# Kernel optimization log

Hardware: AMD Instinct MI355X
Metric: run time of the kernel (lower is better)

## Reference

```python
import jax, jax.numpy as jnp
import numpy as np

C_IN = 256
C_BN = 64


def conv1x1(x, w, b):
    # x: [B, Cin, H, W], w: [Cout, Cin], b: [Cout] -> [B, Cout, H, W]
    return jnp.einsum('oc,bchw->bohw', w, x) + b[None, :, None, None]


def setup_inputs() -> dict:
    key = jax.random.key(0)
    ks = jax.random.split(key, 9)
    B, H, W = 4, 64, 64
    s_in = 1.0 / np.sqrt(C_IN)
    s_bn = 1.0 / np.sqrt(C_BN)
    return {
        'x': jax.random.normal(ks[0], (B, C_IN, H, W), jnp.float32),
        'w_k': jax.random.uniform(ks[1], (C_BN, C_IN), jnp.float32, -s_in, s_in),
        'b_k': jax.random.uniform(ks[2], (C_BN,), jnp.float32, -s_in, s_in),
        'w_q': jax.random.uniform(ks[3], (C_BN, C_IN), jnp.float32, -s_in, s_in),
        'b_q': jax.random.uniform(ks[4], (C_BN,), jnp.float32, -s_in, s_in),
        'w_v': jax.random.uniform(ks[5], (C_BN, C_IN), jnp.float32, -s_in, s_in),
        'b_v': jax.random.uniform(ks[6], (C_BN,), jnp.float32, -s_in, s_in),
        'w_u': jax.random.uniform(ks[7], (C_IN, C_BN), jnp.float32, -s_bn, s_bn),
        'b_u': jax.random.uniform(ks[8], (C_IN,), jnp.float32, -s_bn, s_bn),
    }


def reference(x, w_k, b_k, w_q, b_q, w_v, b_v, w_u, b_u):
    B, C, H, W = x.shape
    N = H * W
    xk = conv1x1(x, w_k, b_k).reshape(B, C_BN, N)            # [B, d, N]
    xq = conv1x1(x, w_q, b_q).reshape(B, C_BN, N)            # [B, d, N]
    xv = conv1x1(x, w_v, b_v).reshape(B, C_BN, N)            # [B, d, N]
    qk = jnp.einsum('bdi,bdk->bik', xq, xk)                  # [B, N, N]
    attn = jax.nn.softmax(qk, axis=2)                        # softmax over keys
    out = jnp.einsum('bik,bdk->bdi', attn, xv)               # [B, d, N]
    out = out.reshape(B, C_BN, H, W)
    y = conv1x1(out, w_u, b_u)                               # [B, C, H, W]
    return x + y
```

## Files before the change

### kernel.cpp

```cpp
#include <hip/hip_runtime.h>
#include <hip/hip_bf16.h>
#include <math.h>

#define N_TOK 4096
#define CIN 256
#define CBN 64
#define LOG2E 1.44269504f

typedef __attribute__((ext_vector_type(8))) short bf16x8;
typedef __attribute__((ext_vector_type(4))) float f32x4;

static __device__ __forceinline__ unsigned short f2bf(float f) {
    union { float f; unsigned u; } v; v.f = f;
    unsigned r = v.u + 0x7fffu + ((v.u >> 16) & 1u);
    return (unsigned short)(r >> 16);
}
static __device__ __forceinline__ unsigned pack2(float a, float b) {
    float2 t2; t2.x = a; t2.y = b;
    __hip_bfloat162 h = __float22bfloat162_rn(t2);
    union { __hip_bfloat162 h; unsigned u; } cv; cv.h = h;
    return cv.u;
}

__global__ __launch_bounds__(256) void prep_w(
        const float* __restrict__ wq, const float* __restrict__ wk,
        const float* __restrict__ wv, const float* __restrict__ wu,
        const float* __restrict__ bq,
        short* __restrict__ Wb, short* __restrict__ Wu, float* __restrict__ bqs) {
    int idx = blockIdx.x * 256 + threadIdx.x;
    int d = idx >> 8, c = idx & 255;
    Wb[d * 256 + c]         = (short)f2bf(wq[idx] * LOG2E);
    Wb[(64 + d) * 256 + c]  = (short)f2bf(wk[idx]);
    Wb[(128 + d) * 256 + c] = (short)f2bf(wv[idx]);
    Wu[idx] = (short)f2bf(wu[idx]);
    if (idx < 64) bqs[idx] = bq[idx] * LOG2E;
}

__global__ __launch_bounds__(256) void qkv_kernel(
        const float* __restrict__ x, const short* __restrict__ Wb,
        const float* __restrict__ bqs, const float* __restrict__ bk, const float* __restrict__ bv,
        short* __restrict__ Qt, short* __restrict__ Kt, short* __restrict__ Vd) {
    int t = threadIdx.x;
    int blk = blockIdx.x;
    int b = blk >> 7;
    int n0 = (blk & 127) * 32;

    __shared__ short Xs[32][264];

    {
        int tok4 = t & 7;
        int cb = t >> 3;
        const float* xb = x + (size_t)b * CIN * N_TOK + n0 + tok4 * 4;
        #pragma unroll
        for (int p = 0; p < 8; ++p) {
            int c = p * 32 + cb;
            float4 xv = *(const float4*)(xb + (size_t)c * N_TOK);
            float xs[4] = {xv.x, xv.y, xv.z, xv.w};
            #pragma unroll
            for (int i = 0; i < 4; ++i)
                Xs[tok4 * 4 + i][c] = (short)f2bf(xs[i]);
        }
    }
    __syncthreads();

    int w = t >> 6;
    int g = (t >> 4) & 3;
    int lr = t & 15;

    f32x4 acc[3][2];
    #pragma unroll
    for (int m = 0; m < 3; ++m)
        #pragma unroll
        for (int st = 0; st < 2; ++st) acc[m][st] = (f32x4){0.f, 0.f, 0.f, 0.f};
    const short* wbase = Wb + (size_t)(w * 16 + lr) * 256 + 8 * g;
    #pragma unroll
    for (int ks = 0; ks < 8; ++ks) {
        bf16x8 xf0 = *(const bf16x8*)&Xs[lr][ks * 32 + 8 * g];
        bf16x8 xf1 = *(const bf16x8*)&Xs[16 + lr][ks * 32 + 8 * g];
        #pragma unroll
        for (int m = 0; m < 3; ++m) {
            bf16x8 wf = *(const bf16x8*)(wbase + (size_t)m * 64 * 256 + ks * 32);
            acc[m][0] = __builtin_amdgcn_mfma_f32_16x16x32_bf16(wf, xf0, acc[m][0], 0, 0, 0);
            acc[m][1] = __builtin_amdgcn_mfma_f32_16x16x32_bf16(wf, xf1, acc[m][1], 0, 0, 0);
        }
    }
    int d0 = w * 16 + 4 * g;
    float4 bq4 = *(const float4*)(bqs + d0);
    float4 bk4 = *(const float4*)(bk + d0);
    float4 bv4 = *(const float4*)(bv + d0);
    float bvr[4] = {bv4.x, bv4.y, bv4.z, bv4.w};
    #pragma unroll
    for (int st = 0; st < 2; ++st) {
        int tok = n0 + st * 16 + lr;
        size_t qo = ((size_t)b * N_TOK + tok) * 64 + d0;
        uint2 qp, kp;
        qp.x = pack2(acc[0][st][0] + bq4.x, acc[0][st][1] + bq4.y);
        qp.y = pack2(acc[0][st][2] + bq4.z, acc[0][st][3] + bq4.w);
        kp.x = pack2(acc[1][st][0] + bk4.x, acc[1][st][1] + bk4.y);
        kp.y = pack2(acc[1][st][2] + bk4.z, acc[1][st][3] + bk4.w);
        *(uint2*)(Qt + qo) = qp;
        *(uint2*)(Kt + qo) = kp;
        int u = tok & 31;
        int vcol = (tok & ~31) + 8 * ((u >> 2) & 3) + 4 * (u >> 4) + (u & 3);
        #pragma unroll
        for (int r = 0; r < 4; ++r)
            Vd[((size_t)b * 64 + d0 + r) * N_TOK + vcol] = (short)f2bf(acc[2][st][r] + bvr[r]);
    }
}

__global__ __launch_bounds__(1024, 4) void attn_out_kernel(
        const short* __restrict__ Qt, const short* __restrict__ Kt,
        const short* __restrict__ Vsw, const short* __restrict__ Wu,
        const float* __restrict__ bu, const float* __restrict__ x,
        float* __restrict__ y) {
    int t = threadIdx.x;
    int w = t >> 6;
    int wq = w >> 3;
    int sp = w & 7;
    int g = (t >> 4) & 3;
    int lr = t & 15;
    int l = t & 63;

    int bid = blockIdx.x;
    int blk = ((bid & 7) << 5) | (bid >> 3);
    int b = blk >> 6;
    int q0 = (blk & 63) * 64;

    const short* Qb = Qt + (size_t)b * N_TOK * 64;
    const short* Kb = Kt + (size_t)b * N_TOK * 64;
    const short* Vb = Vsw + (size_t)b * 64 * N_TOK;

    __shared__ __align__(16) char LB[8][2][8192];
    __shared__ float Ml[32][16];
    __shared__ __align__(16) short Olds[64 * 64];

    bf16x8 qf[2][2];
    #pragma unroll
    for (int j = 0; j < 2; ++j) {
        const short* qp = Qb + (q0 + (wq * 2 + j) * 16 + lr) * 64 + 8 * g;
        qf[j][0] = *(const bf16x8*)qp;
        qf[j][1] = *(const bf16x8*)(qp + 32);
    }

    f32x4 o[2][4];
    #pragma unroll
    for (int j = 0; j < 2; ++j)
        #pragma unroll
        for (int mt = 0; mt < 4; ++mt) o[j][mt] = (f32x4){0.f, 0.f, 0.f, 0.f};
    float la0 = 0.f, la1 = 0.f;

    int krow = l >> 3;
    int kchk = ((l & 7) ^ krow) * 8;
    int vrow = l >> 2;
    int vchk = ((l & 3) ^ (vrow & 3)) * 8;

    auto STAGE = [&](int kt, int buf) {
        int k0s = sp * 512 + kt * 32;
        char* dst0 = &LB[sp][buf][0];
        if (wq == 0) {
            #pragma unroll
            for (int j = 0; j < 4; ++j) {
                const short* src = Kb + (size_t)(k0s + j * 8 + krow) * 64 + kchk;
                __builtin_amdgcn_global_load_lds(
                    (const __attribute__((address_space(1))) void*)src,
                    (__attribute__((address_space(3))) void*)(dst0 + j * 1024),
                    16, 0, 0);
            }
        } else {
            #pragma unroll
            for (int j = 0; j < 4; ++j) {
                const short* src = Vb + (size_t)(j * 16 + vrow) * N_TOK + k0s + vchk;
                __builtin_amdgcn_global_load_lds(
                    (const __attribute__((address_space(1))) void*)src,
                    (__attribute__((address_space(3))) void*)(dst0 + 4096 + j * 1024),
                    16, 0, 0);
            }
        }
    };

    STAGE(0, 0);
    __syncthreads();

    int cK = (g ^ (lr & 7)) << 4;
    int cV = (g ^ (lr & 3)) << 4;
    int cur = 0;
    for (int kt = 0; kt < 16; ++kt) {
        if (kt < 15) STAGE(kt + 1, cur ^ 1);
        const char* KB_ = &LB[sp][cur][0];
        const char* VB_ = KB_ + 4096;
        f32x4 s[2][2];
        #pragma unroll
        for (int nt = 0; nt < 2; ++nt) {
            const char* rp = KB_ + (nt * 16 + lr) * 128;
            bf16x8 kf0 = *(const bf16x8*)(rp + cK);
            bf16x8 kf1 = *(const bf16x8*)(rp + (cK ^ 64));
            #pragma unroll
            for (int j = 0; j < 2; ++j) {
                f32x4 z = (f32x4){0.f, 0.f, 0.f, 0.f};
                z = __builtin_amdgcn_mfma_f32_16x16x32_bf16(kf0, qf[j][0], z, 0, 0, 0);
                s[j][nt] = __builtin_amdgcn_mfma_f32_16x16x32_bf16(kf1, qf[j][1], z, 0, 0, 0);
            }
        }
        #pragma unroll
        for (int nt = 0; nt < 2; ++nt)
            #pragma unroll
            for (int r = 0; r < 4; ++r) {
                float p0 = __builtin_amdgcn_exp2f(s[0][nt][r]);
                float p1 = __builtin_amdgcn_exp2f(s[1][nt][r]);
                s[0][nt][r] = p0; la0 += p0;
                s[1][nt][r] = p1; la1 += p1;
            }
        union { bf16x8 v; unsigned u[4]; } b0u, b1u;
        b0u.u[0] = pack2(s[0][0][0], s[0][0][1]);
        b0u.u[1] = pack2(s[0][0][2], s[0][0][3]);
        b0u.u[2] = pack2(s[0][1][0], s[0][1][1]);
        b0u.u[3] = pack2(s[0][1][2], s[0][1][3]);
        b1u.u[0] = pack2(s[1][0][0], s[1][0][1]);
        b1u.u[1] = pack2(s[1][0][2], s[1][0][3]);
        b1u.u[2] = pack2(s[1][1][0], s[1][1][1]);
        b1u.u[3] = pack2(s[1][1][2], s[1][1][3]);
        #pragma unroll
        for (int mt = 0; mt < 4; ++mt) {
            bf16x8 av = *(const bf16x8*)(VB_ + (mt * 16 + lr) * 64 + cV);
            o[0][mt] = __builtin_amdgcn_mfma_f32_16x16x32_bf16(av, b0u.v, o[0][mt], 0, 0, 0);
            o[1][mt] = __builtin_amdgcn_mfma_f32_16x16x32_bf16(av, b1u.v, o[1][mt], 0, 0, 0);
        }
        __syncthreads();
        cur ^= 1;
    }
    la0 += __shfl_xor(la0, 16); la0 += __shfl_xor(la0, 32);
    la1 += __shfl_xor(la1, 16); la1 += __shfl_xor(la1, 32);
    float* OmL = (float*)&LB[0][0][0];
    #pragma unroll
    for (int j = 0; j < 2; ++j) {
        int qt = wq * 2 + j;
        #pragma unroll
        for (int mt = 0; mt < 4; ++mt)
            *(f32x4*)(OmL + ((qt * 8 + sp) * 16 + lr) * 64 + mt * 16 + 4 * g) = o[j][mt];
        Ml[qt * 8 + sp][lr] = j == 0 ? la0 : la1;
    }
    __syncthreads();
    {
        int qt2 = t >> 8, q = (t >> 4) & 15, dq = t & 15;
        float a0 = 0.f, a1 = 0.f, a2 = 0.f, a3 = 0.f, lsum = 0.f;
        #pragma unroll
        for (int s2 = 0; s2 < 8; ++s2) {
            const float* pp = OmL + ((qt2 * 8 + s2) * 16 + q) * 64 + dq * 4;
            float4 v = *(const float4*)pp;
            a0 += v.x; a1 += v.y; a2 += v.z; a3 += v.w;
            lsum += Ml[qt2 * 8 + s2][q];
        }
        float inv = 1.f / lsum;
        int tau = qt2 * 16 + q;
        uint2 ow;
        ow.x = pack2(a0 * inv, a1 * inv);
        ow.y = pack2(a2 * inv, a3 * inv);
        char* dst = (char*)Olds + tau * 128 + (((dq >> 1) ^ (tau & 7)) << 4) + (dq & 1) * 8;
        *(uint2*)dst = ow;
    }
    __syncthreads();
    {
        int tt = w & 3;
        int cq = w >> 2;
        int tau = tt * 16 + lr;
        const char* orow = (const char*)Olds + tau * 128;
        bf16x8 a0 = *(const bf16x8*)(orow + ((g ^ (lr & 7)) << 4));
        bf16x8 a1 = *(const bf16x8*)(orow + (((4 + g) ^ (lr & 7)) << 4));
        #pragma unroll
        for (int ct = 0; ct < 4; ++ct) {
            int c = cq * 64 + ct * 16 + lr;
            const short* wp = Wu + (size_t)c * 64 + 8 * g;
            bf16x8 b0 = *(const bf16x8*)wp;
            bf16x8 b1 = *(const bf16x8*)(wp + 32);
            f32x4 acc = (f32x4){0.f, 0.f, 0.f, 0.f};
            acc = __builtin_amdgcn_mfma_f32_16x16x32_bf16(a0, b0, acc, 0, 0, 0);
            acc = __builtin_amdgcn_mfma_f32_16x16x32_bf16(a1, b1, acc, 0, 0, 0);
            float bc = bu[c];
            size_t base = ((size_t)b * CIN + c) * N_TOK + q0 + tt * 16 + 4 * g;
            float4 xr = *(const float4*)(x + base);
            float4 yo;
            yo.x = acc[0] + bc + xr.x;
            yo.y = acc[1] + bc + xr.y;
            yo.z = acc[2] + bc + xr.z;
            yo.w = acc[3] + bc + xr.w;
            *(float4*)(y + base) = yo;
        }
    }
}

extern "C" void kernel_launch(void* const* d_in, const int* in_sizes, int n_in,
                              void* d_out, int out_size, void* d_ws, size_t ws_size,
                              hipStream_t stream) {
    const float* x  = (const float*)d_in[0];
    const float* wk = (const float*)d_in[1];
    const float* bk = (const float*)d_in[2];
    const float* wq = (const float*)d_in[3];
    const float* bq = (const float*)d_in[4];
    const float* wv = (const float*)d_in[5];
    const float* bv = (const float*)d_in[6];
    const float* wu = (const float*)d_in[7];
    const float* bu = (const float*)d_in[8];
    float* out = (float*)d_out;

    char* ws = (char*)d_ws;
    if (ws_size < (size_t)(7u << 20)) return;
    short* Qt  = (short*)(ws);
    short* Kt  = (short*)(ws + (2u << 20));
    short* Vd  = (short*)(ws + (4u << 20));
    short* Wb  = (short*)(ws + (6u << 20));
    short* Wu  = Wb + 192 * 256;
    float* bqs = (float*)(Wu + 256 * 64);

    prep_w<<<dim3(64), dim3(256), 0, stream>>>(wq, wk, wv, wu, bq, Wb, Wu, bqs);
    qkv_kernel<<<dim3(512), dim3(256), 0, stream>>>(x, Wb, bqs, bk, bv, Qt, Kt, Vd);
    attn_out_kernel<<<dim3(256), dim3(1024), 0, stream>>>(Qt, Kt, Vd, Wu, bu, x, out);
}
```

Before: 58.78 us.

## Split attention over key halves into separate blocks with merge-and-project kernel

The fused attention+projection kernel of 1024 threads is split into an attention kernel of 512-thread blocks, each handling one query tile over half the keys, so twice as many blocks run. Partial unnormalized outputs are stored as bf16 with their row sums, and a new merge kernel adds the two halves, normalizes, and applies the up-projection plus residual. The LDS partial-output layout is also swizzled to reduce bank conflicts. In exchange this adds a kernel launch, extra global traffic for the partials, and a further bf16 rounding of the unnormalized partial outputs.

```diff
diff --git a/kernel.cpp b/kernel.cpp
--- a/kernel.cpp
+++ b/kernel.cpp
@@ -20,6 +20,12 @@
     __hip_bfloat162 h = __float22bfloat162_rn(t2);
     union { __hip_bfloat162 h; unsigned u; } cv; cv.h = h;
     return cv.u;
+}
+static __device__ __forceinline__ float bflo(unsigned u) {
+    union { unsigned u; float f; } c; c.u = (u & 0xffffu) << 16; return c.f;
+}
+static __device__ __forceinline__ float bfhi(unsigned u) {
+    union { unsigned u; float f; } c; c.u = u & 0xffff0000u; return c.f;
 }
 
 __global__ __launch_bounds__(256) void prep_w(
@@ -108,31 +114,32 @@
     }
 }
 
-__global__ __launch_bounds__(1024, 4) void attn_out_kernel(
+__global__ __launch_bounds__(512, 4) void attn_half_kernel(
         const short* __restrict__ Qt, const short* __restrict__ Kt,
-        const short* __restrict__ Vsw, const short* __restrict__ Wu,
-        const float* __restrict__ bu, const float* __restrict__ x,
-        float* __restrict__ y) {
+        const short* __restrict__ Vsw, short* __restrict__ Oh,
+        float* __restrict__ lh) {
     int t = threadIdx.x;
     int w = t >> 6;
-    int wq = w >> 3;
-    int sp = w & 7;
+    int wq = w >> 2;
+    int sp = w & 3;
     int g = (t >> 4) & 3;
     int lr = t & 15;
     int l = t & 63;
 
     int bid = blockIdx.x;
-    int blk = ((bid & 7) << 5) | (bid >> 3);
-    int b = blk >> 6;
-    int q0 = (blk & 63) * 64;
+    int swz = ((bid & 7) << 6) | (bid >> 3);
+    int b = swz >> 7;
+    int rem = swz & 127;
+    int q0 = (rem >> 1) * 64;
+    int half = rem & 1;
+    int kbase = half * 2048;
 
     const short* Qb = Qt + (size_t)b * N_TOK * 64;
     const short* Kb = Kt + (size_t)b * N_TOK * 64;
     const short* Vb = Vsw + (size_t)b * 64 * N_TOK;
 
-    __shared__ __align__(16) char LB[8][2][8192];
-    __shared__ float Ml[32][16];
-    __shared__ __align__(16) short Olds[64 * 64];
+    __shared__ __align__(16) char LB[4][2][8192];
+    __shared__ float Ml[16][16];
 
     bf16x8 qf[2][2];
     #pragma unroll
@@ -155,7 +162,7 @@
     int vchk = ((l & 3) ^ (vrow & 3)) * 8;
 
     auto STAGE = [&](int kt, int buf) {
-        int k0s = sp * 512 + kt * 32;
+        int k0s = kbase + sp * 512 + kt * 32;
         char* dst0 = &LB[sp][buf][0];
         if (wq == 0) {
             #pragma unroll
@@ -234,41 +241,86 @@
     #pragma unroll
     for (int j = 0; j < 2; ++j) {
         int qt = wq * 2 + j;
-        #pragma unroll
-        for (int mt = 0; mt < 4; ++mt)
-            *(f32x4*)(OmL + ((qt * 8 + sp) * 16 + lr) * 64 + mt * 16 + 4 * g) = o[j][mt];
-        Ml[qt * 8 + sp][lr] = j == 0 ? la0 : la1;
+        int row = (qt * 4 + sp) * 16 + lr;
+        #pragma unroll
+        for (int mt = 0; mt < 4; ++mt) {
+            int c = mt * 4 + g;
+            int cs = (c & 8) | ((c & 7) ^ (lr & 7));
+            *(f32x4*)(OmL + (size_t)row * 64 + cs * 4) = o[j][mt];
+        }
+        Ml[qt * 4 + sp][lr] = j == 0 ? la0 : la1;
     }
     __syncthreads();
     {
-        int qt2 = t >> 8, q = (t >> 4) & 15, dq = t & 15;
-        float a0 = 0.f, a1 = 0.f, a2 = 0.f, a3 = 0.f, lsum = 0.f;
-        #pragma unroll
-        for (int s2 = 0; s2 < 8; ++s2) {
-            const float* pp = OmL + ((qt2 * 8 + s2) * 16 + q) * 64 + dq * 4;
-            float4 v = *(const float4*)pp;
-            a0 += v.x; a1 += v.y; a2 += v.z; a3 += v.w;
-            lsum += Ml[qt2 * 8 + s2][q];
-        }
-        float inv = 1.f / lsum;
+        int qt2 = t >> 7;
+        int q = (t >> 3) & 15;
+        int dh = t & 7;
+        int dq0 = dh * 2, dq1 = dq0 + 1;
+        int cs0 = (dq0 & 8) | ((dq0 & 7) ^ (q & 7));
+        int cs1 = (dq1 & 8) | ((dq1 & 7) ^ (q & 7));
+        f32x4 a0 = (f32x4){0.f,0.f,0.f,0.f}, a1 = (f32x4){0.f,0.f,0.f,0.f};
+        float lsum = 0.f;
+        #pragma unroll
+        for (int s2 = 0; s2 < 4; ++s2) {
+            int row = (qt2 * 4 + s2) * 16 + q;
+            f32x4 v0 = *(const f32x4*)(OmL + (size_t)row * 64 + cs0 * 4);
+            f32x4 v1 = *(const f32x4*)(OmL + (size_t)row * 64 + cs1 * 4);
+            a0 += v0; a1 += v1;
+            lsum += Ml[qt2 * 4 + s2][q];
+        }
+        int tok = q0 + qt2 * 16 + q;
+        uint4 ow;
+        ow.x = pack2(a0[0], a0[1]);
+        ow.y = pack2(a0[2], a0[3]);
+        ow.z = pack2(a1[0], a1[1]);
+        ow.w = pack2(a1[2], a1[3]);
+        *(uint4*)(Oh + ((size_t)(half * 4 + b) * N_TOK + tok) * 64 + dh * 8) = ow;
+        if (dh == 0) lh[(size_t)(half * 4 + b) * N_TOK + tok] = lsum;
+    }
+}
+
+__global__ __launch_bounds__(512, 4) void mergeup_kernel(
+        const short* __restrict__ Oh, const float* __restrict__ lh,
+        const short* __restrict__ Wu, const float* __restrict__ bu,
+        const float* __restrict__ x, float* __restrict__ y) {
+    int t = threadIdx.x;
+    int blk = blockIdx.x;
+    int b = blk >> 6;
+    int q0 = (blk & 63) * 64;
+
+    __shared__ __align__(16) short Olds[64 * 64];
+
+    {
+        int qt2 = t >> 7, q = (t >> 3) & 15, dh = t & 7;
+        int tok = q0 + qt2 * 16 + q;
+        size_t o0 = ((size_t)b * N_TOK + tok) * 64 + dh * 8;
+        size_t o1 = ((size_t)(4 + b) * N_TOK + tok) * 64 + dh * 8;
+        uint4 u0 = *(const uint4*)(Oh + o0);
+        uint4 u1 = *(const uint4*)(Oh + o1);
+        float inv = 1.f / (lh[(size_t)b * N_TOK + tok] + lh[(size_t)(4 + b) * N_TOK + tok]);
+        unsigned uu0[4] = {u0.x, u0.y, u0.z, u0.w};
+        unsigned uu1[4] = {u1.x, u1.y, u1.z, u1.w};
+        unsigned outw[4];
+        #pragma unroll
+        for (int i = 0; i < 4; ++i)
+            outw[i] = pack2((bflo(uu0[i]) + bflo(uu1[i])) * inv,
+                            (bfhi(uu0[i]) + bfhi(uu1[i])) * inv);
         int tau = qt2 * 16 + q;
-        uint2 ow;
-        ow.x = pack2(a0 * inv, a1 * inv);
-        ow.y = pack2(a2 * inv, a3 * inv);
-        char* dst = (char*)Olds + tau * 128 + (((dq >> 1) ^ (tau & 7)) << 4) + (dq & 1) * 8;
-        *(uint2*)dst = ow;
+        uint4 ow; ow.x = outw[0]; ow.y = outw[1]; ow.z = outw[2]; ow.w = outw[3];
+        *(uint4*)((char*)Olds + tau * 128 + ((dh ^ (tau & 7)) << 4)) = ow;
     }
     __syncthreads();
     {
+        int w = t >> 6, g = (t >> 4) & 3, lr = t & 15;
         int tt = w & 3;
-        int cq = w >> 2;
+        int ch = w >> 2;
         int tau = tt * 16 + lr;
         const char* orow = (const char*)Olds + tau * 128;
-        bf16x8 a0 = *(const bf16x8*)(orow + ((g ^ (lr & 7)) << 4));
-        bf16x8 a1 = *(const bf16x8*)(orow + (((4 + g) ^ (lr & 7)) << 4));
-        #pragma unroll
-        for (int ct = 0; ct < 4; ++ct) {
-            int c = cq * 64 + ct * 16 + lr;
+        bf16x8 a0 = *(const bf16x8*)(orow + ((g ^ (tau & 7)) << 4));
+        bf16x8 a1 = *(const bf16x8*)(orow + (((4 + g) ^ (tau & 7)) << 4));
+        #pragma unroll
+        for (int ct = 0; ct < 8; ++ct) {
+            int c = ch * 128 + ct * 16 + lr;
             const short* wp = Wu + (size_t)c * 64 + 8 * g;
             bf16x8 b0 = *(const bf16x8*)wp;
             bf16x8 b1 = *(const bf16x8*)(wp + 32);
@@ -303,15 +355,18 @@
     float* out = (float*)d_out;
 
     char* ws = (char*)d_ws;
-    if (ws_size < (size_t)(7u << 20)) return;
+    if (ws_size < (size_t)10748160u) return;
     short* Qt  = (short*)(ws);
-    short* Kt  = (short*)(ws + (2u << 20));
-    short* Vd  = (short*)(ws + (4u << 20));
-    short* Wb  = (short*)(ws + (6u << 20));
-    short* Wu  = Wb + 192 * 256;
-    float* bqs = (float*)(Wu + 256 * 64);
+    short* Kt  = (short*)(ws + 2097152u);
+    short* Vd  = (short*)(ws + 4194304u);
+    short* Oh  = (short*)(ws + 6291456u);
+    float* lh  = (float*)(ws + 10485760u);
+    short* Wb  = (short*)(ws + 10616832u);
+    short* Wu  = (short*)(ws + 10715136u);
+    float* bqs = (float*)(ws + 10747904u);
 
     prep_w<<<dim3(64), dim3(256), 0, stream>>>(wq, wk, wv, wu, bq, Wb, Wu, bqs);
     qkv_kernel<<<dim3(512), dim3(256), 0, stream>>>(x, Wb, bqs, bk, bv, Qt, Kt, Vd);
-    attn_out_kernel<<<dim3(256), dim3(1024), 0, stream>>>(Qt, Kt, Vd, Wu, bu, x, out);
-}
+    attn_half_kernel<<<dim3(512), dim3(512), 0, stream>>>(Qt, Kt, Vd, Oh, lh);
+    mergeup_kernel<<<dim3(256), dim3(512), 0, stream>>>(Oh, lh, Wu, bu, x, out);
+}
```

Result: faster. 56.06 us (-4.6%).
